# Kernel tuning notes

Hardware: AMD Instinct MI355X
Metric: run time of the kernel (lower is better)

## Reference

```python
import jax, jax.numpy as jnp
import numpy as np

# dims (see shape_source)
N = 20000      # spots / graph nodes
G = 3000       # genes
NF = 256       # NFeature = CrossAttention dim
D_IN = 256     # dims_spot[0]
HID = 64       # dims_spot[1]
OUT = 16       # dims_spot[2]
H = 3          # GATv2 heads
E1 = 640000
E2 = 320000
SLOPE = 0.2    # leaky relu negative slope (GATv2 + CrossAttention alpha)


def _gat_params(key, din, hid, heads):
    k = jax.random.split(key, 3)
    s = 1.0 / np.sqrt(din)
    Wl = jax.random.normal(k[0], (din, heads * hid), jnp.float32) * s
    Wr = jax.random.normal(k[1], (din, heads * hid), jnp.float32) * s
    att = jax.random.normal(k[2], (heads, hid), jnp.float32) * s
    bl = jnp.zeros((heads * hid,), jnp.float32)
    br = jnp.zeros((heads * hid,), jnp.float32)
    b = jnp.zeros((hid,), jnp.float32)
    return Wl, bl, Wr, br, att, b


def setup_inputs() -> dict:
    key = jax.random.key(0)
    ks = jax.random.split(key, 16)
    inp = {
        "gene_freq_mtx": jax.random.normal(ks[0], (NF, G), jnp.float32),
        "gene_eigvecs_T": jax.random.normal(ks[1], (G, N), jnp.float32) / np.sqrt(G),
        "spot_freq_mtx": jax.random.normal(ks[2], (N, D_IN), jnp.float32),
        "spot_eigvecs_T": jax.random.normal(ks[3], (D_IN, NF), jnp.float32) / np.sqrt(D_IN),
        "spotnet": jax.random.randint(ks[4], (2, E1), 0, N, jnp.int32),
        "spotnet_cluster": jax.random.randint(ks[5], (2, E2), 0, N, jnp.int32),
    }
    for name, din, kk in [("c1", D_IN, ks[6]), ("c1p", D_IN, ks[7]), ("c3", OUT, ks[8]), ("c3p", OUT, ks[9])]:
        Wl, bl, Wr, br, att, b = _gat_params(kk, din, HID, H)
        inp[name + "_Wl"] = Wl; inp[name + "_bl"] = bl
        inp[name + "_Wr"] = Wr; inp[name + "_br"] = br
        inp[name + "_att"] = att; inp[name + "_b"] = b
    inp["W2"] = jax.random.normal(ks[10], (2 * HID, OUT), jnp.float32) / np.sqrt(2 * HID)
    inp["b2"] = jnp.zeros((OUT,), jnp.float32)
    inp["W4"] = jax.random.normal(ks[11], (2 * HID, D_IN), jnp.float32) / np.sqrt(2 * HID)
    inp["b4"] = jnp.zeros((D_IN,), jnp.float32)
    inp["a1"] = jax.random.normal(ks[12], (2 * NF, 1), jnp.float32) * 0.05
    inp["a2"] = jax.random.normal(ks[13], (2 * NF, 1), jnp.float32) * 0.05
    return inp


def gatv2(x, edge_index, Wl, bl, Wr, br, att, b, n):
    """PyG GATv2Conv, concat=False (head mean), add_self_loops=False, eval mode."""
    heads, c = att.shape
    src, dst = edge_index[0], edge_index[1]
    xl = (x @ Wl + bl).reshape(-1, heads, c)   # source transform [N,H,C]
    xr = (x @ Wr + br).reshape(-1, heads, c)   # target transform [N,H,C]
    m = jax.nn.leaky_relu(xl[src] + xr[dst], SLOPE)          # [E,H,C]
    e = jnp.einsum('ehc,hc->eh', m, att)                      # [E,H]
    emax = jax.ops.segment_max(e, dst, num_segments=n)        # [N,H]
    emax = jnp.where(jnp.isfinite(emax), emax, 0.0)           # empty segments
    p = jnp.exp(e - emax[dst])
    denom = jax.ops.segment_sum(p, dst, num_segments=n)       # [N,H]
    alpha = p / jnp.maximum(denom, 1e-16)[dst]                # segment softmax
    out = jax.ops.segment_sum(alpha[:, :, None] * xl[src], dst, num_segments=n)
    return out.mean(axis=1) + b                                # [N,C]


def reference(gene_freq_mtx, gene_eigvecs_T, spot_freq_mtx, spot_eigvecs_T,
              c1_Wl, c1_bl, c1_Wr, c1_br, c1_att, c1_b,
              c1p_Wl, c1p_bl, c1p_Wr, c1p_br, c1p_att, c1p_b,
              W2, b2,
              c3_Wl, c3_bl, c3_Wr, c3_br, c3_att, c3_b,
              c3p_Wl, c3p_bl, c3p_Wr, c3p_br, c3p_att, c3p_b,
              W4, b4, a1, a2, spotnet, spotnet_cluster):
    n = spot_freq_mtx.shape[0]
    # GAT (cluster=True)
    h1n = gatv2(spot_freq_mtx, spotnet, c1_Wl, c1_bl, c1_Wr, c1_br, c1_att, c1_b, n)
    h1p = gatv2(spot_freq_mtx, spotnet_cluster, c1p_Wl, c1p_bl, c1p_Wr, c1p_br, c1p_att, c1p_b, n)
    h1 = jax.nn.elu(jnp.concatenate([h1n, h1p], axis=1))
    h2 = h1 @ W2 + b2                                          # emb_spot [N,OUT]
    h3n = gatv2(h2, spotnet, c3_Wl, c3_bl, c3_Wr, c3_br, c3_att, c3_b, n)
    h3p = gatv2(h2, spotnet_cluster, c3p_Wl, c3p_bl, c3p_Wr, c3p_br, c3p_att, c3p_b, n)
    h3 = jax.nn.elu(jnp.concatenate([h3n, h3p], axis=1))
    h4 = h3 @ W4 + b4                                          # mtx_res_spot [N,D_IN]
    # iGFT + clip-at-zero (== relu)
    Xg = jax.nn.relu(gene_eigvecs_T.T @ gene_freq_mtx.T)       # [N,NF]
    Xs = jax.nn.relu(h4 @ spot_eigvecs_T)                      # [N,NF]
    # CrossAttention (dropout=0.0)
    cat = jnp.concatenate([Xg, Xs], axis=1)                    # [N,2NF]
    e = jax.nn.leaky_relu(jnp.concatenate([cat @ a1, cat @ a2], axis=1), SLOPE)
    lam = jax.nn.softmax(e, axis=1)                            # [N,2]
    res = lam[:, :1] * Xg + lam[:, 1:] * Xs
    return (res, lam, h2, h4)
```

## Files before the change

### kernel.cpp

```cpp
#include <hip/hip_runtime.h>

typedef unsigned short u16;
typedef __attribute__((ext_vector_type(8))) short bf16x8;
typedef __attribute__((ext_vector_type(4))) float floatx4;

#define NSPOT 20000
#define NGENE 3000
#define E1N   640000
#define E2N   320000

#define OFF_RES 0
#define OFF_LAM 5120000
#define OFF_H2  5160000
#define OFF_H4  5480000

__device__ __forceinline__ float b2f(u16 u){
  union { unsigned int i; float f; } v; v.i = ((unsigned int)u) << 16; return v.f;
}
__device__ __forceinline__ u16 f2b(float f){
  union { float f; unsigned int i; } v; v.f = f;
  unsigned int i = v.i;
  return (u16)((i + 0x7FFFu + ((i >> 16) & 1u)) >> 16);
}
__device__ __forceinline__ void stout(void* O, size_t i, float v, int isbf){
  if (isbf) ((u16*)O)[i] = f2b(v); else ((float*)O)[i] = v;
}
__device__ __forceinline__ u16 ldu(const void* p, size_t i, int isbf){
  return isbf ? ((const u16*)p)[i] : f2b(((const float*)p)[i]);
}

__global__ void sniff_kernel(const u16* __restrict__ x, int* __restrict__ flag){
  int lane = threadIdx.x;
  u16 u = x[lane * 2];
  int e = (u >> 7) & 0xFF;
  int sane = (u == 0) || (e >= 0x60 && e <= 0xA0);
  unsigned long long b = __ballot(sane);
  if (lane == 0) flag[0] = (__popcll(b) >= 48) ? 1 : 0;
}

struct ConvSeg { const void* src; u16* dst; int n; };
struct ConvBatch { ConvSeg s[14]; };
__global__ void convbatch_kernel(ConvBatch cb, const int* __restrict__ dflag){
  ConvSeg S = cb.s[blockIdx.y];
  int i = blockIdx.x * 256 + threadIdx.x;
  if (i < S.n) S.dst[i] = ldu(S.src, i, dflag[0]);
}

__global__ void conv3_kernel(const void* __restrict__ s0, u16* __restrict__ d0, int n0,
                             const void* __restrict__ s1, u16* __restrict__ d1, int n1,
                             const void* __restrict__ s2, u16* __restrict__ d2, int n2,
                             const int* __restrict__ dflag){
  int i = blockIdx.x * 256 + threadIdx.x;
  const void* src; u16* dst; int local;
  if (i < n0){ src = s0; dst = d0; local = i; }
  else if (i < n0 + n1){ src = s1; dst = d1; local = i - n0; }
  else if (i < n0 + n1 + n2){ src = s2; dst = d2; local = i - n0 - n1; }
  else return;
  size_t b = (size_t)local * 4;
  u16 o[4];
  if (dflag[0]){
    *(uint2*)o = *(const uint2*)((const u16*)src + b);
  } else {
    float4 f = *(const float4*)((const float*)src + b);
    o[0]=f2b(f.x); o[1]=f2b(f.y); o[2]=f2b(f.z); o[3]=f2b(f.w);
  }
  *(uint2*)(dst + b) = *(uint2*)o;
}

__global__ void hist2_kernel(const int* __restrict__ dst0, int E0, int* __restrict__ cnt0,
                             const int* __restrict__ dst1, int E1, int* __restrict__ cnt1){
  const int* dst = blockIdx.y ? dst1 : dst0;
  int* cnt = blockIdx.y ? cnt1 : cnt0;
  int E = blockIdx.y ? E1 : E0;
  int e = blockIdx.x * 256 + threadIdx.x;
  if (e < E){ int d = dst[e]; if ((unsigned)d < (unsigned)NSPOT) atomicAdd(&cnt[d], 1); }
}

__global__ void scan2_kernel(const int* __restrict__ c0, int* __restrict__ o0, int* __restrict__ u0,
                             const int* __restrict__ c1, int* __restrict__ o1, int* __restrict__ u1,
                             int n){
  const int* cnt = blockIdx.x ? c1 : c0;
  int* off = blockIdx.x ? o1 : o0;
  int* cur = blockIdx.x ? u1 : u0;
  __shared__ int part[256];
  int tid = threadIdx.x;
  int chunk = (n + 255) / 256;
  int lo = tid * chunk; if (lo > n) lo = n;
  int hi = lo + chunk; if (hi > n) hi = n;
  int s = 0;
  for (int i = lo; i < hi; i++) s += cnt[i];
  part[tid] = s;
  __syncthreads();
  if (tid == 0){
    int run = 0;
    for (int i = 0; i < 256; i++){ int t = part[i]; part[i] = run; run += t; }
  }
  __syncthreads();
  int run = part[tid];
  for (int i = lo; i < hi; i++){ off[i] = run; cur[i] = run; run += cnt[i]; }
  if (hi == n) off[n] = run;
}

__global__ void scatter2_kernel(const int* __restrict__ src0, const int* __restrict__ dst0,
                                int* __restrict__ cur0, int* __restrict__ out0, int E0,
                                const int* __restrict__ src1, const int* __restrict__ dst1,
                                int* __restrict__ cur1, int* __restrict__ out1, int E1){
  const int* src = blockIdx.y ? src1 : src0;
  const int* dst = blockIdx.y ? dst1 : dst0;
  int* cur = blockIdx.y ? cur1 : cur0;
  int* out = blockIdx.y ? out1 : out0;
  int E = blockIdx.y ? E1 : E0;
  int e = blockIdx.x * 256 + threadIdx.x;
  if (e < E){
    int d = dst[e];
    if ((unsigned)d < (unsigned)NSPOT){
      int p = atomicAdd(&cur[d], 1);
      if ((unsigned)p < (unsigned)E) out[p] = src[e];
    }
  }
}

struct AsmSet {
  const void *Wl, *bl, *Wr, *br, *Wlp, *blp, *Wrp, *brp;
  u16* Wcat; u16* bcat; int Kdim;
};
__global__ void assemble2_kernel(AsmSet s0, AsmSet s1, const int* __restrict__ dflag){
  AsmSet S = blockIdx.y ? s1 : s0;
  int isbf = dflag[0];
  int idx = blockIdx.x * 256 + threadIdx.x;
  int total = S.Kdim * 768;
  if (idx < total){
    int k = idx / 768, j = idx % 768;
    int seg = j / 192, jj = j % 192;
    const void* W = (seg == 0) ? S.Wl : (seg == 1) ? S.Wr : (seg == 2) ? S.Wlp : S.Wrp;
    S.Wcat[idx] = ldu(W, (size_t)k * 192 + jj, isbf);
  }
  if (idx < 768){
    int seg = idx / 192, jj = idx % 192;
    const void* b = (seg == 0) ? S.bl : (seg == 1) ? S.br : (seg == 2) ? S.blp : S.brp;
    S.bcat[idx] = ldu(b, jj, isbf);
  }
}

__global__ __launch_bounds__(256) void xg_kernel(
    const u16* __restrict__ GF,
    const void* __restrict__ GE,
    u16* __restrict__ XG,
    const int* __restrict__ dflag)
{
  constexpr int KC = 128;
  constexpr int LDA = KC + 8;
  __shared__ __align__(16) u16 As[256 * LDA];
  const int isbf = dflag[0];
  const float* GE32 = (const float*)GE;
  const u16*   GE16 = (const u16*)GE;
  int tid = threadIdx.x;
  int lane = tid & 63, w = tid >> 6;
  int quad = lane >> 4, c16 = lane & 15;
  int n = blockIdx.x * 64 + w * 16 + c16;
  int nc = min(n, NSPOT - 1);
  floatx4 acc[16] = {};
  const int NCH = (NGENE + KC - 1) / KC;
  for (int ch = 0; ch < NCH; ch++){
    int k0 = ch * KC;
    {
      const u16* src = GF + (size_t)tid * NGENE + k0;
      u16* dst = &As[tid * LDA];
#pragma unroll
      for (int i = 0; i < KC / 8; i++){
        if (k0 + i * 8 + 8 <= NGENE){
          *(uint4*)(dst + i * 8) = *(const uint4*)(src + i * 8);
        } else {
          for (int e = 0; e < 8; e++)
            dst[i * 8 + e] = (k0 + i * 8 + e < NGENE) ? src[i * 8 + e] : (u16)0;
        }
      }
    }
    __syncthreads();
#pragma unroll
    for (int s = 0; s < KC / 32; s++){
      u16 bfr[8];
#pragma unroll
      for (int j = 0; j < 8; j++){
        int k = k0 + s * 32 + quad * 8 + j;
        int kcl = min(k, NGENE - 1);
        float bv = isbf ? b2f(GE16[(size_t)kcl * NSPOT + nc])
                        : GE32[(size_t)kcl * NSPOT + nc];
        bfr[j] = f2b(bv);
      }
      bf16x8 bv8 = *(bf16x8*)bfr;
#pragma unroll
      for (int mt = 0; mt < 16; mt++){
        bf16x8 av = *(const bf16x8*)&As[(mt * 16 + c16) * LDA + s * 32 + quad * 8];
        acc[mt] = __builtin_amdgcn_mfma_f32_16x16x32_bf16(av, bv8, acc[mt], 0, 0, 0);
      }
    }
    __syncthreads();
  }
  if (n < NSPOT){
    u16* row = XG + (size_t)n * 256;
#pragma unroll
    for (int mt = 0; mt < 16; mt++){
      u16 o[4];
#pragma unroll
      for (int r = 0; r < 4; r++) o[r] = f2b(fmaxf(acc[mt][r], 0.f));
      *(uint2*)(row + mt * 16 + quad * 4) = *(uint2*)o;
    }
  }
}

template<int BMI, bool A_KM, bool B_NK, bool A_EXT, bool B_EXT, bool RELU, bool HAS_BIAS, bool C_OUT, bool C2>
__global__ __launch_bounds__(256) void gemm_mfma(
    const void* __restrict__ A, const void* __restrict__ B,
    const u16* __restrict__ bias, void* __restrict__ Cp, u16* __restrict__ Cp2,
    const int* __restrict__ dflag, size_t aoff, size_t coff,
    int M, int N, int K, int lda, int ldb, int ldc, int ldc2)
{
  const int isbf = dflag[0];
  constexpr int BM = 64 * BMI, BK = 32, LDA = BK + 8, LDB = BK + 8;
  __shared__ __align__(16) u16 As[BM * LDA];
  __shared__ __align__(16) u16 Bs[64 * LDB];
  const u16*   A16 = (const u16*)A + aoff;
  const float* A32 = (const float*)A + aoff;
  const u16*   B16 = (const u16*)B;
  const float* B32 = (const float*)B;
  auto ldA = [&](size_t i) -> u16 { return (!A_EXT || isbf) ? A16[i] : f2b(A32[i]); };
  auto ldB = [&](size_t i) -> u16 { return (!B_EXT || isbf) ? B16[i] : f2b(B32[i]); };

  int tid = threadIdx.x;
  int lane = tid & 63, w = tid >> 6;
  int m0 = blockIdx.y * BM, n0 = blockIdx.x * 64;
  floatx4 acc[BMI][4] = {};
  int quad = lane >> 4;
  int nk = (K + BK - 1) / BK;
  for (int kt = 0; kt < nk; kt++){
    int k0 = kt * BK;
    if (!A_KM){
#pragma unroll
      for (int i = 0; i < BMI; i++){
        int id = tid + i * 256;
        int r = id >> 2, c = (id & 3) * 8;
        int gm = m0 + r, gk = k0 + c;
        if (gm < M && gk + 8 <= K){
          if (!A_EXT || isbf){
            *(uint4*)&As[r * LDA + c] = *(const uint4*)(A16 + (size_t)gm * lda + gk);
          } else {
            const float* p = A32 + (size_t)gm * lda + gk;
            float4 f0 = *(const float4*)p, f1 = *(const float4*)(p + 4);
            u16* d = &As[r * LDA + c];
            d[0]=f2b(f0.x); d[1]=f2b(f0.y); d[2]=f2b(f0.z); d[3]=f2b(f0.w);
            d[4]=f2b(f1.x); d[5]=f2b(f1.y); d[6]=f2b(f1.z); d[7]=f2b(f1.w);
          }
        } else {
          for (int e = 0; e < 8; e++)
            As[r * LDA + c + e] = (gm < M && gk + e < K) ? ldA((size_t)gm * lda + gk + e) : (u16)0;
        }
      }
    } else {
#pragma unroll
      for (int i = 0; i < BMI; i++){
        int id = tid + i * 256;
        int kk, rr;
        if (BMI == 2){ kk = id >> 4; rr = (id & 15) * 8; }
        else         { kk = id >> 3; rr = (id & 7) * 8; }
        int gk = k0 + kk, gm = m0 + rr;
        if (gk < K && gm + 8 <= M){
          if (!A_EXT || isbf){
            uint4 v = *(const uint4*)(A16 + (size_t)gk * lda + gm);
            const u16* pv = (const u16*)&v;
#pragma unroll
            for (int e = 0; e < 8; e++) As[(rr + e) * LDA + kk] = pv[e];
          } else {
            const float* p = A32 + (size_t)gk * lda + gm;
            float4 f0 = *(const float4*)p, f1 = *(const float4*)(p + 4);
            As[(rr+0)*LDA+kk]=f2b(f0.x); As[(rr+1)*LDA+kk]=f2b(f0.y);
            As[(rr+2)*LDA+kk]=f2b(f0.z); As[(rr+3)*LDA+kk]=f2b(f0.w);
            As[(rr+4)*LDA+kk]=f2b(f1.x); As[(rr+5)*LDA+kk]=f2b(f1.y);
            As[(rr+6)*LDA+kk]=f2b(f1.z); As[(rr+7)*LDA+kk]=f2b(f1.w);
          }
        } else {
          for (int e = 0; e < 8; e++)
            As[(rr + e) * LDA + kk] = (gk < K && gm + e < M) ? ldA((size_t)gk * lda + gm + e) : (u16)0;
        }
      }
    }
    if (B_NK){
      int r = tid >> 2, c = (tid & 3) * 8;
      int gn = n0 + r, gk = k0 + c;
      if (gn < N && gk + 8 <= K){
        if (!B_EXT || isbf){
          *(uint4*)&Bs[r * LDB + c] = *(const uint4*)(B16 + (size_t)gn * ldb + gk);
        } else {
          const float* p = B32 + (size_t)gn * ldb + gk;
          float4 f0 = *(const float4*)p, f1 = *(const float4*)(p + 4);
          u16* d = &Bs[r * LDB + c];
          d[0]=f2b(f0.x); d[1]=f2b(f0.y); d[2]=f2b(f0.z); d[3]=f2b(f0.w);
          d[4]=f2b(f1.x); d[5]=f2b(f1.y); d[6]=f2b(f1.z); d[7]=f2b(f1.w);
        }
      } else {
        for (int e = 0; e < 8; e++)
          Bs[r * LDB + c + e] = (gn < N && gk + e < K) ? ldB((size_t)gn * ldb + gk + e) : (u16)0;
      }
    } else {
      int kk = tid >> 3, nn = (tid & 7) * 8;
      int gk = k0 + kk, gn = n0 + nn;
      if (gk < K && gn + 8 <= N){
        if (!B_EXT || isbf){
          uint4 v = *(const uint4*)(B16 + (size_t)gk * ldb + gn);
          const u16* pv = (const u16*)&v;
#pragma unroll
          for (int e = 0; e < 8; e++) Bs[(nn + e) * LDB + kk] = pv[e];
        } else {
          const float* p = B32 + (size_t)gk * ldb + gn;
          float4 f0 = *(const float4*)p, f1 = *(const float4*)(p + 4);
          Bs[(nn+0)*LDB+kk]=f2b(f0.x); Bs[(nn+1)*LDB+kk]=f2b(f0.y);
          Bs[(nn+2)*LDB+kk]=f2b(f0.z); Bs[(nn+3)*LDB+kk]=f2b(f0.w);
          Bs[(nn+4)*LDB+kk]=f2b(f1.x); Bs[(nn+5)*LDB+kk]=f2b(f1.y);
          Bs[(nn+6)*LDB+kk]=f2b(f1.z); Bs[(nn+7)*LDB+kk]=f2b(f1.w);
        }
      } else {
        for (int e = 0; e < 8; e++)
          Bs[(nn + e) * LDB + kk] = (gk < K && gn + e < N) ? ldB((size_t)gk * ldb + gn + e) : (u16)0;
      }
    }
    __syncthreads();
    bf16x8 af[BMI];
#pragma unroll
    for (int mi = 0; mi < BMI; mi++)
      af[mi] = *(const bf16x8*)&As[(w * (16 * BMI) + mi * 16 + (lane & 15)) * LDA + quad * 8];
#pragma unroll
    for (int ni = 0; ni < 4; ni++){
      bf16x8 bfr = *(const bf16x8*)&Bs[(ni * 16 + (lane & 15)) * LDB + quad * 8];
#pragma unroll
      for (int mi = 0; mi < BMI; mi++)
        acc[mi][ni] = __builtin_amdgcn_mfma_f32_16x16x32_bf16(af[mi], bfr, acc[mi][ni], 0, 0, 0);
    }
    __syncthreads();
  }
#pragma unroll
  for (int mi = 0; mi < BMI; mi++)
#pragma unroll
    for (int ni = 0; ni < 4; ni++)
#pragma unroll
      for (int r = 0; r < 4; r++){
        int row = m0 + w * (16 * BMI) + mi * 16 + quad * 4 + r;
        int col = n0 + ni * 16 + (lane & 15);
        if (row < M && col < N){
          float v = acc[mi][ni][r];
          if (HAS_BIAS) v += b2f(bias[col]);
          if (RELU) v = fmaxf(v, 0.f);
          size_t ci = coff + (size_t)row * ldc + col;
          if (!C_OUT) ((u16*)Cp)[ci] = f2b(v);
          else stout(Cp, ci, v, isbf);
          if (C2) Cp2[(size_t)row * ldc2 + col] = f2b(v);
        }
      }
}

struct GatSet {
  const int* off; const int* srcs; const u16* att; const u16* bias;
  int xl_off, xr_off, out_off, E;
};
__global__ __launch_bounds__(256) void gat2_kernel(
    const u16* __restrict__ Y, GatSet SA, GatSet SB,
    u16* __restrict__ aggout, int n)
{
  int half = gridDim.x >> 1;
  int selB = (int)blockIdx.x >= half;
  GatSet S = selB ? SB : SA;
  int bx = blockIdx.x - (selB ? half : 0);
  int wid = (bx * 256 + threadIdx.x) >> 6;
  int lane = threadIdx.x & 63;
  if (wid >= n) return;
  int sub = lane >> 3;
  int cbase = (lane & 7) * 8;
  const int ldY = 768;
  size_t drow = (size_t)wid * ldY;

  float xr[3][8], at[3][8];
#pragma unroll
  for (int h = 0; h < 3; h++){
    uint4 vx = *(const uint4*)(Y + drow + S.xr_off + h * 64 + cbase);
    uint4 va = *(const uint4*)(S.att + h * 64 + cbase);
    const u16* px = (const u16*)&vx;
    const u16* pa = (const u16*)&va;
#pragma unroll
    for (int j = 0; j < 8; j++){ xr[h][j] = b2f(px[j]); at[h][j] = b2f(pa[j]); }
  }

  int beg = S.off[wid], end = S.off[wid + 1];
  beg = max(0, min(beg, S.E));
  end = max(beg, min(end, S.E));

  float mh[3] = {-INFINITY, -INFINITY, -INFINITY};
  float lh[3] = {0.f, 0.f, 0.f};
  float ac[3][8] = {};

  uint4 xa[3] = {};
  int s_b = 0;
  if (beg < end){
    int e0 = beg + sub;
    int s = (e0 < end) ? S.srcs[e0] : 0;
    if ((unsigned)s >= (unsigned)NSPOT) s = 0;
    const u16* p = Y + (size_t)s * ldY + S.xl_off + cbase;
#pragma unroll
    for (int h = 0; h < 3; h++) xa[h] = *(const uint4*)(p + h * 64);
    if (beg + 8 < end){
      int e1 = beg + 8 + sub;
      int s1 = (e1 < end) ? S.srcs[e1] : 0;
      if ((unsigned)s1 >= (unsigned)NSPOT) s1 = 0;
      s_b = s1;
    }
  }

  for (int b = beg; b < end; b += 8){
    uint4 xc[3];
#pragma unroll
    for (int h = 0; h < 3; h++) xc[h] = xa[h];
    bool act = (b + sub) < end;

    if (b + 8 < end){
      const u16* p = Y + (size_t)s_b * ldY + S.xl_off + cbase;
#pragma unroll
      for (int h = 0; h < 3; h++) xa[h] = *(const uint4*)(p + h * 64);
      if (b + 16 < end){
        int e2 = b + 16 + sub;
        int s2 = (e2 < end) ? S.srcs[e2] : 0;
        if ((unsigned)s2 >= (unsigned)NSPOT) s2 = 0;
        s_b = s2;
      }
    }

    float xl[3][8];
    float t0 = 0.f, t1 = 0.f, t2 = 0.f;
    {
      const u16* p0 = (const u16*)&xc[0];
      const u16* p1 = (const u16*)&xc[1];
      const u16* p2 = (const u16*)&xc[2];
#pragma unroll
      for (int j = 0; j < 8; j++){
        float x0 = b2f(p0[j]); xl[0][j] = x0;
        float u0 = x0 + xr[0][j]; u0 = fmaxf(u0, 0.2f * u0);
        t0 = __builtin_fmaf(at[0][j], u0, t0);
        float x1 = b2f(p1[j]); xl[1][j] = x1;
        float u1 = x1 + xr[1][j]; u1 = fmaxf(u1, 0.2f * u1);
        t1 = __builtin_fmaf(at[1][j], u1, t1);
        float x2 = b2f(p2[j]); xl[2][j] = x2;
        float u2 = x2 + xr[2][j]; u2 = fmaxf(u2, 0.2f * u2);
        t2 = __builtin_fmaf(at[2][j], u2, t2);
      }
    }
#pragma unroll
    for (int d = 1; d < 8; d <<= 1){
      t0 += __shfl_xor(t0, d, 64);
      t1 += __shfl_xor(t1, d, 64);
      t2 += __shfl_xor(t2, d, 64);
    }
    if (act){
      float tt[3] = {t0, t1, t2};
#pragma unroll
      for (int h = 0; h < 3; h++){
        float nm = fmaxf(mh[h], tt[h]);
        if (nm > mh[h]){
          float sc = __expf(mh[h] - nm);
          lh[h] *= sc;
#pragma unroll
          for (int j = 0; j < 8; j++) ac[h][j] *= sc;
          mh[h] = nm;
        }
        float w = __expf(tt[h] - mh[h]);
        lh[h] += w;
#pragma unroll
        for (int j = 0; j < 8; j++) ac[h][j] = __builtin_fmaf(w, xl[h][j], ac[h][j]);
      }
    }
  }

  float o[8] = {};
#pragma unroll
  for (int h = 0; h < 3; h++){
    float gm = fmaxf(mh[h], __shfl_xor(mh[h], 8, 64));
    gm = fmaxf(gm, __shfl_xor(gm, 16, 64));
    gm = fmaxf(gm, __shfl_xor(gm, 32, 64));
    float sc = (mh[h] == -INFINITY) ? 0.f : __expf(mh[h] - gm);
    float L = lh[h] * sc;
    L += __shfl_xor(L, 8, 64);
    L += __shfl_xor(L, 16, 64);
    L += __shfl_xor(L, 32, 64);
    float inv = 1.f / fmaxf(L, 1e-16f);
#pragma unroll
    for (int j = 0; j < 8; j++){
      float a = ac[h][j] * sc;
      a += __shfl_xor(a, 8, 64);
      a += __shfl_xor(a, 16, 64);
      a += __shfl_xor(a, 32, 64);
      o[j] += a * inv;
    }
  }
  if (sub == 0){
    u16 ov[8];
#pragma unroll
    for (int j = 0; j < 8; j++){
      float v = o[j] * (1.f / 3.f) + b2f(S.bias[cbase + j]);
      v = (v > 0.f) ? v : expm1f(v);
      if (!(fabsf(v) < 1e30f)) v = 0.f;
      ov[j] = f2b(v);
    }
    *(uint4*)&aggout[(size_t)wid * 128 + S.out_off + cbase] = *(uint4*)ov;
  }
}

__global__ __launch_bounds__(256) void h2y2_kernel(
    const u16* __restrict__ AGG, const u16* __restrict__ W2, const u16* __restrict__ b2,
    const u16* __restrict__ Wcat2, const u16* __restrict__ bcat2,
    void* __restrict__ OUT, u16* __restrict__ Y2,
    const int* __restrict__ dflag, int n){
  __shared__ float w2s[128 * 16];
  __shared__ float as_[16][128];
  __shared__ float h[16][16];
  __shared__ __align__(16) u16 ws_[16 * 768];
  int isbf = dflag[0];
  int tid = threadIdx.x;
  for (int i = tid; i < 128 * 16; i += 256) w2s[i] = b2f(W2[i]);
  for (int i = tid; i < 1536; i += 256) ((uint4*)ws_)[i] = ((const uint4*)Wcat2)[i];
  int m0 = blockIdx.x * 16;
  for (int i = tid; i < 16 * 128; i += 256){
    int r = i >> 7, c = i & 127; int m = m0 + r;
    as_[r][c] = (m < n) ? b2f(AGG[(size_t)m * 128 + c]) : 0.f;
  }
  __syncthreads();
  {
    int r = tid >> 4, j = tid & 15;
    int m = m0 + r;
    float acc = b2f(b2[j]);
    for (int k = 0; k < 128; k++) acc += as_[r][k] * w2s[k * 16 + j];
    h[r][j] = acc;
    if (m < n) stout(OUT, (size_t)OFF_H2 + (size_t)m * 16 + j, acc, isbf);
  }
  __syncthreads();
  int j = tid;
  float acc[16][3];
  float bj0 = b2f(bcat2[j]), bj1 = b2f(bcat2[j + 256]), bj2 = b2f(bcat2[j + 512]);
#pragma unroll
  for (int r = 0; r < 16; r++){ acc[r][0] = bj0; acc[r][1] = bj1; acc[r][2] = bj2; }
  for (int k = 0; k < 16; k++){
    float w0 = b2f(ws_[k * 768 + j]);
    float w1 = b2f(ws_[k * 768 + j + 256]);
    float w2 = b2f(ws_[k * 768 + j + 512]);
#pragma unroll
    for (int r = 0; r < 16; r++){
      float hv = h[r][k];
      acc[r][0] += hv * w0; acc[r][1] += hv * w1; acc[r][2] += hv * w2;
    }
  }
#pragma unroll
  for (int r = 0; r < 16; r++){
    int m = m0 + r;
    if (m < n){
      size_t base = (size_t)m * 768;
      Y2[base + j] = f2b(acc[r][0]);
      Y2[base + j + 256] = f2b(acc[r][1]);
      Y2[base + j + 512] = f2b(acc[r][2]);
    }
  }
}

__global__ __launch_bounds__(256) void cross_attn_kernel(
    const u16* __restrict__ XG, const u16* __restrict__ XS,
    const u16* __restrict__ a1, const u16* __restrict__ a2,
    void* __restrict__ OUT, const int* __restrict__ dflag, int n){
  int wid = (blockIdx.x * 256 + threadIdx.x) >> 6;
  int lane = threadIdx.x & 63;
  if (wid >= n) return;
  int isbf = dflag[0];
  int c0 = lane * 4;
  size_t base = (size_t)wid * 256 + c0;
  float g[4], s[4];
#pragma unroll
  for (int e = 0; e < 4; e++){ g[e] = b2f(XG[base + e]); s[e] = b2f(XS[base + e]); }
  float p1 = 0.f, p2 = 0.f;
#pragma unroll
  for (int e = 0; e < 4; e++){
    p1 += g[e] * b2f(a1[c0 + e]) + s[e] * b2f(a1[256 + c0 + e]);
    p2 += g[e] * b2f(a2[c0 + e]) + s[e] * b2f(a2[256 + c0 + e]);
  }
#pragma unroll
  for (int d = 32; d > 0; d >>= 1){
    p1 += __shfl_xor(p1, d, 64);
    p2 += __shfl_xor(p2, d, 64);
  }
  float e1 = (p1 > 0.f) ? p1 : 0.2f * p1;
  float e2 = (p2 > 0.f) ? p2 : 0.2f * p2;
  float mx = fmaxf(e1, e2);
  float w1 = __expf(e1 - mx), w2 = __expf(e2 - mx);
  float inv = 1.f / (w1 + w2);
  float l0 = w1 * inv, l1 = w2 * inv;
#pragma unroll
  for (int e = 0; e < 4; e++)
    stout(OUT, (size_t)OFF_RES + base + e, l0 * g[e] + l1 * s[e], isbf);
  if (lane == 0){
    stout(OUT, (size_t)OFF_LAM + (size_t)wid * 2,     l0, isbf);
    stout(OUT, (size_t)OFF_LAM + (size_t)wid * 2 + 1, l1, isbf);
  }
}

extern "C" void kernel_launch(void* const* d_in, const int* in_sizes, int n_in,
                              void* d_out, int out_size, void* d_ws, size_t ws_size,
                              hipStream_t stream) {
  const void* gene_freq = d_in[0];
  const void* gene_eig  = d_in[1];
  const void* spot_freq = d_in[2];
  const void* spot_eig  = d_in[3];
  const int* net1 = (const int*)d_in[4];
  const int* net2 = (const int*)d_in[5];
  const void *c1_Wl=d_in[6],  *c1_bl=d_in[7],  *c1_Wr=d_in[8],  *c1_br=d_in[9],  *c1_att=d_in[10], *c1_b=d_in[11];
  const void *c1p_Wl=d_in[12],*c1p_bl=d_in[13],*c1p_Wr=d_in[14],*c1p_br=d_in[15],*c1p_att=d_in[16],*c1p_b=d_in[17];
  const void *c3_Wl=d_in[18], *c3_bl=d_in[19], *c3_Wr=d_in[20], *c3_br=d_in[21], *c3_att=d_in[22], *c3_b=d_in[23];
  const void *c3p_Wl=d_in[24],*c3p_bl=d_in[25],*c3p_Wr=d_in[26],*c3p_br=d_in[27],*c3p_att=d_in[28],*c3p_b=d_in[29];
  const void *W2=d_in[30], *b2=d_in[31], *W4=d_in[32], *b4=d_in[33], *a1=d_in[34], *a2=d_in[35];

  char* p0 = (char*)d_ws;
  char* p = p0;
  auto carve = [&](size_t bytes) -> char* {
    char* r = p; p += (bytes + 255) & ~(size_t)255; return r;
  };
  int*   flag  = (int*) carve(256);
  int*   cnt1  = (int*) carve((NSPOT + 2) * 4);
  int*   off1  = (int*) carve((NSPOT + 2) * 4);
  int*   cur1  = (int*) carve((NSPOT + 2) * 4);
  int*   srcs1 = (int*) carve((size_t)E1N * 4);
  int*   cnt2  = (int*) carve((NSPOT + 2) * 4);
  int*   off2  = (int*) carve((NSPOT + 2) * 4);
  int*   cur2  = (int*) carve((NSPOT + 2) * 4);
  int*   srcs2 = (int*) carve((size_t)E2N * 4);
  u16*   Wcat1 = (u16*) carve(256 * 768 * 2);
  u16*   bcat1 = (u16*) carve(2048);
  u16*   Wcat2 = (u16*) carve(16 * 768 * 2);
  u16*   bcat2 = (u16*) carve(2048);
  u16*   attc1  = (u16*)carve(192 * 2);
  u16*   attc1p = (u16*)carve(192 * 2);
  u16*   attc3  = (u16*)carve(192 * 2);
  u16*   attc3p = (u16*)carve(192 * 2);
  u16*   bc1  = (u16*)carve(64 * 2);
  u16*   bc1p = (u16*)carve(64 * 2);
  u16*   bc3  = (u16*)carve(64 * 2);
  u16*   bc3p = (u16*)carve(64 * 2);
  u16*   W2c  = (u16*)carve(2048 * 2);
  u16*   b2c  = (u16*)carve(16 * 2);
  u16*   W4c  = (u16*)carve(32768 * 2);
  u16*   b4c  = (u16*)carve(256 * 2);
  u16*   a1c  = (u16*)carve(512 * 2);
  u16*   a2c  = (u16*)carve(512 * 2);
  u16*   GF16 = (u16*) carve((size_t)256 * 3000 * 2);
  u16*   SE16 = (u16*) carve((size_t)256 * 256 * 2);
  u16*   SF16 = (u16*) carve((size_t)NSPOT * 256 * 2);
  u16*   H4B  = (u16*) carve((size_t)NSPOT * 256 * 2);
  u16*   AGG  = (u16*) carve((size_t)NSPOT * 128 * 2);
  u16*   XG   = (u16*) carve((size_t)NSPOT * 256 * 2);
  char*  R    = carve((size_t)2 * 256 * NSPOT * 4);
  u16*   Y    = (u16*)R;
  u16*   XS   = (u16*)(R + (size_t)NSPOT * 768 * 2);

  sniff_kernel<<<1, 64, 0, stream>>>((const u16*)spot_freq, flag);
  hipMemsetAsync(cnt1, 0, NSPOT * 4, stream);
  hipMemsetAsync(cnt2, 0, NSPOT * 4, stream);
  hist2_kernel<<<dim3((E1N + 255) / 256, 2), 256, 0, stream>>>(
      net1 + E1N, E1N, cnt1, net2 + E2N, E2N, cnt2);
  scan2_kernel<<<2, 256, 0, stream>>>(cnt1, off1, cur1, cnt2, off2, cur2, NSPOT);
  scatter2_kernel<<<dim3((E1N + 255) / 256, 2), 256, 0, stream>>>(
      net1, net1 + E1N, cur1, srcs1, E1N, net2, net2 + E2N, cur2, srcs2, E2N);

  ConvBatch cb;
  cb.s[0]  = {c1_att,  attc1,  192}; cb.s[1]  = {c1p_att, attc1p, 192};
  cb.s[2]  = {c3_att,  attc3,  192}; cb.s[3]  = {c3p_att, attc3p, 192};
  cb.s[4]  = {c1_b, bc1, 64}; cb.s[5]  = {c1p_b, bc1p, 64};
  cb.s[6]  = {c3_b, bc3, 64}; cb.s[7]  = {c3p_b, bc3p, 64};
  cb.s[8]  = {W2, W2c, 2048}; cb.s[9]  = {b2, b2c, 16};
  cb.s[10] = {W4, W4c, 32768}; cb.s[11] = {b4, b4c, 256};
  cb.s[12] = {a1, a1c, 512}; cb.s[13] = {a2, a2c, 512};
  convbatch_kernel<<<dim3(128, 14), 256, 0, stream>>>(cb, flag);

  {
    int n0 = 256 * 3000 / 4, n1 = 256 * 256 / 4, n2 = NSPOT * 256 / 4;
    int tot = n0 + n1 + n2;
    conv3_kernel<<<(tot + 255) / 256, 256, 0, stream>>>(
        gene_freq, GF16, n0, spot_eig, SE16, n1, spot_freq, SF16, n2, flag);
  }

  AsmSet as0 = {c1_Wl, c1_bl, c1_Wr, c1_br, c1p_Wl, c1p_bl, c1p_Wr, c1p_br, Wcat1, bcat1, 256};
  AsmSet as1 = {c3_Wl, c3_bl, c3_Wr, c3_br, c3p_Wl, c3p_bl, c3p_Wr, c3p_br, Wcat2, bcat2, 16};
  assemble2_kernel<<<dim3((256 * 768 + 255) / 256, 2), 256, 0, stream>>>(as0, as1, flag);

  GatSet g1a = {off1, srcs1, attc1,  bc1,  0,   192, 0,  E1N};
  GatSet g1b = {off2, srcs2, attc1p, bc1p, 384, 576, 64, E2N};
  GatSet g3a = {off1, srcs1, attc3,  bc3,  0,   192, 0,  E1N};
  GatSet g3b = {off2, srcs2, attc3p, bc3p, 384, 576, 64, E2N};

  xg_kernel<<<313, 256, 0, stream>>>(GF16, gene_eig, XG, flag);

  gemm_mfma<2, false, false, false, false, false, true, false, false>
      <<<dim3(12, 157), 256, 0, stream>>>(
      SF16, Wcat1, bcat1, Y, nullptr, flag, 0, 0,
      NSPOT, 768, 256, 256, 768, 768, 0);
  gat2_kernel<<<10000, 256, 0, stream>>>(Y, g1a, g1b, AGG, NSPOT);
  h2y2_kernel<<<1250, 256, 0, stream>>>(AGG, W2c, b2c, Wcat2, bcat2, d_out, Y, flag, NSPOT);
  gat2_kernel<<<10000, 256, 0, stream>>>(Y, g3a, g3b, AGG, NSPOT);
  gemm_mfma<1, false, false, false, false, false, true, true, true>
      <<<dim3(4, 313), 256, 0, stream>>>(
      AGG, W4c, b4c, d_out, H4B, flag, 0, OFF_H4,
      NSPOT, 256, 128, 128, 256, 256, 256);
  gemm_mfma<1, false, false, false, false, true, false, false, false>
      <<<dim3(4, 313), 256, 0, stream>>>(
      H4B, SE16, nullptr, XS, nullptr, flag, 0, 0,
      NSPOT, 256, 256, 256, 256, 256, 0);
  cross_attn_kernel<<<5000, 256, 0, stream>>>(XG, XS, a1c, a2c, d_out, flag, NSPOT);

  (void)in_sizes; (void)n_in; (void)out_size; (void)ws_size;
}
```

Before: 1.102 ms.

## Split-K the XG gene GEMM across four chunks with a separate reduction kernel

The XG kernel previously ran only 313 blocks, each looping over all 3000 genes. It now splits K into four 768-wide chunks on a second grid dimension, writes fp32 partial sums to a scratch buffer, and a new kernel sums the partials, applies relu and converts to bf16. The intent is to quadruple parallelism on a GPU with many CUs. The cost is roughly 80MB of extra fp32 partial traffic plus one more launch. The K tile also shrinks to 64, and the bf16 path skips the float round-trip.

```diff
diff --git a/kernel.cpp b/kernel.cpp
--- a/kernel.cpp
+++ b/kernel.cpp
@@ -145,11 +145,12 @@
 __global__ __launch_bounds__(256) void xg_kernel(
     const u16* __restrict__ GF,
     const void* __restrict__ GE,
-    u16* __restrict__ XG,
+    float* __restrict__ P,
     const int* __restrict__ dflag)
 {
-  constexpr int KC = 128;
+  constexpr int KC = 64;
   constexpr int LDA = KC + 8;
+  constexpr int KCHUNK = 768;
   __shared__ __align__(16) u16 As[256 * LDA];
   const int isbf = dflag[0];
   const float* GE32 = (const float*)GE;
@@ -159,20 +160,21 @@
   int quad = lane >> 4, c16 = lane & 15;
   int n = blockIdx.x * 64 + w * 16 + c16;
   int nc = min(n, NSPOT - 1);
+  int z = blockIdx.y;
+  int kbeg = z * KCHUNK;
+  int kend = min(kbeg + KCHUNK, NGENE);
   floatx4 acc[16] = {};
-  const int NCH = (NGENE + KC - 1) / KC;
-  for (int ch = 0; ch < NCH; ch++){
-    int k0 = ch * KC;
+  for (int k0 = kbeg; k0 < kend; k0 += KC){
     {
       const u16* src = GF + (size_t)tid * NGENE + k0;
       u16* dst = &As[tid * LDA];
 #pragma unroll
       for (int i = 0; i < KC / 8; i++){
-        if (k0 + i * 8 + 8 <= NGENE){
+        if (k0 + i * 8 + 8 <= kend){
           *(uint4*)(dst + i * 8) = *(const uint4*)(src + i * 8);
         } else {
           for (int e = 0; e < 8; e++)
-            dst[i * 8 + e] = (k0 + i * 8 + e < NGENE) ? src[i * 8 + e] : (u16)0;
+            dst[i * 8 + e] = (k0 + i * 8 + e < kend) ? src[i * 8 + e] : (u16)0;
         }
       }
     }
@@ -180,13 +182,21 @@
 #pragma unroll
     for (int s = 0; s < KC / 32; s++){
       u16 bfr[8];
-#pragma unroll
-      for (int j = 0; j < 8; j++){
-        int k = k0 + s * 32 + quad * 8 + j;
-        int kcl = min(k, NGENE - 1);
-        float bv = isbf ? b2f(GE16[(size_t)kcl * NSPOT + nc])
-                        : GE32[(size_t)kcl * NSPOT + nc];
-        bfr[j] = f2b(bv);
+      int krow = k0 + s * 32 + quad * 8;
+      if (isbf){
+        const u16* gp = GE16 + (size_t)min(krow, NGENE - 1) * NSPOT + nc;
+#pragma unroll
+        for (int j = 0; j < 8; j++){
+          int kcl = min(krow + j, NGENE - 1);
+          bfr[j] = GE16[(size_t)kcl * NSPOT + nc];
+        }
+        (void)gp;
+      } else {
+#pragma unroll
+        for (int j = 0; j < 8; j++){
+          int kcl = min(krow + j, NGENE - 1);
+          bfr[j] = f2b(GE32[(size_t)kcl * NSPOT + nc]);
+        }
       }
       bf16x8 bv8 = *(bf16x8*)bfr;
 #pragma unroll
@@ -198,15 +208,31 @@
     __syncthreads();
   }
   if (n < NSPOT){
-    u16* row = XG + (size_t)n * 256;
+    float* row = P + (size_t)z * NSPOT * 256 + (size_t)n * 256;
 #pragma unroll
     for (int mt = 0; mt < 16; mt++){
-      u16 o[4];
-#pragma unroll
-      for (int r = 0; r < 4; r++) o[r] = f2b(fmaxf(acc[mt][r], 0.f));
-      *(uint2*)(row + mt * 16 + quad * 4) = *(uint2*)o;
-    }
-  }
+      float4 o;
+      o.x = acc[mt][0]; o.y = acc[mt][1]; o.z = acc[mt][2]; o.w = acc[mt][3];
+      *(float4*)(row + mt * 16 + quad * 4) = o;
+    }
+  }
+}
+
+__global__ __launch_bounds__(256) void xgred_kernel(const float* __restrict__ P,
+                                                    u16* __restrict__ XG){
+  size_t i = ((size_t)blockIdx.x * 256 + threadIdx.x) * 4;
+  const size_t ZS = (size_t)NSPOT * 256;
+  if (i >= ZS) return;
+  float4 a = *(const float4*)(P + i);
+  float4 b = *(const float4*)(P + ZS + i);
+  float4 c = *(const float4*)(P + 2 * ZS + i);
+  float4 d = *(const float4*)(P + 3 * ZS + i);
+  u16 o[4];
+  o[0] = f2b(fmaxf(a.x + b.x + c.x + d.x, 0.f));
+  o[1] = f2b(fmaxf(a.y + b.y + c.y + d.y, 0.f));
+  o[2] = f2b(fmaxf(a.z + b.z + c.z + d.z, 0.f));
+  o[3] = f2b(fmaxf(a.w + b.w + c.w + d.w, 0.f));
+  *(uint2*)(XG + i) = *(uint2*)o;
 }
 
 template<int BMI, bool A_KM, bool B_NK, bool A_EXT, bool B_EXT, bool RELU, bool HAS_BIAS, bool C_OUT, bool C2>
@@ -657,7 +683,8 @@
   u16*   H4B  = (u16*) carve((size_t)NSPOT * 256 * 2);
   u16*   AGG  = (u16*) carve((size_t)NSPOT * 128 * 2);
   u16*   XG   = (u16*) carve((size_t)NSPOT * 256 * 2);
-  char*  R    = carve((size_t)2 * 256 * NSPOT * 4);
+  char*  R    = carve((size_t)4 * NSPOT * 256 * 4);
+  float* Pbuf = (float*)R;
   u16*   Y    = (u16*)R;
   u16*   XS   = (u16*)(R + (size_t)NSPOT * 768 * 2);
 
@@ -696,7 +723,8 @@
   GatSet g3a = {off1, srcs1, attc3,  bc3,  0,   192, 0,  E1N};
   GatSet g3b = {off2, srcs2, attc3p, bc3p, 384, 576, 64, E2N};
 
-  xg_kernel<<<313, 256, 0, stream>>>(GF16, gene_eig, XG, flag);
+  xg_kernel<<<dim3(313, 4), 256, 0, stream>>>(GF16, gene_eig, Pbuf, flag);
+  xgred_kernel<<<5000, 256, 0, stream>>>(Pbuf, XG);
 
   gemm_mfma<2, false, false, false, false, false, true, false, false>
       <<<dim3(12, 157), 256, 0, stream>>>(
```

Result: no change. 1.088 ms (-1.3%).
